# Kernel optimization log

Measured on AMD Instinct MI355X. Metric: run time of the kernel, lower is better.

The kernel has to match this reference:

```python
import jax, jax.numpy as jnp
import numpy as np

E, H = 1024, 16
B, N = 4, 2048
D = E // H

def setup_inputs() -> dict:
    key = jax.random.key(0)
    ks = jax.random.split(key, 5)
    s = 1.0 / np.sqrt(E)
    return {
        "x": jax.random.normal(ks[0], (B, N, E), dtype=jnp.float32),
        "Wqkv": jax.random.normal(ks[1], (E, 3 * E), dtype=jnp.float32) * s,
        "bqkv": jnp.zeros((3 * E,), dtype=jnp.float32),
        "Wproj": jax.random.normal(ks[2], (E, E), dtype=jnp.float32) * s,
        "bproj": jnp.zeros((E,), dtype=jnp.float32),
    }

def reference(x, Wqkv, bqkv, Wproj, bproj):
    b, n, e = x.shape
    qkv = x @ Wqkv + bqkv  # [b, n, 3e]
    # torch rearrange 'b n (h d qkv) -> qkv b h n d': last dim splits as (h, d, 3)
    qkv = qkv.reshape(b, n, H, D, 3)
    qkv = jnp.transpose(qkv, (4, 0, 2, 1, 3))  # [3, b, h, n, d]
    q, k, v = qkv[0], qkv[1], qkv[2]
    # NOTE: module scales by 1/sqrt(e) (full embed dim), faithfully reproduced
    att = jax.nn.softmax(jnp.einsum('bhqd,bhkd->bhqk', q, k) / jnp.sqrt(jnp.float32(E)), axis=-1)
    out = jnp.einsum('bhqk,bhkd->bhqd', att, v)  # dropout is identity in eval
    out = jnp.transpose(out, (0, 2, 1, 3)).reshape(b, n, e)  # 'b h n d -> b n (h d)'
    return out @ Wproj + bproj
```

## Files before the change

kernel.cpp:

```cpp
#include <hip/hip_runtime.h>
#include <stdint.h>

typedef unsigned short u16;
typedef __attribute__((ext_vector_type(8))) short short8;
typedef __attribute__((ext_vector_type(4))) float f32x4;

#define LOG2E 1.44269504088896340736f
#define CS (0.03125f * LOG2E)
#define BB 4
#define NN 2048
#define EE 1024
#define HH 16
#define DD 64
#define MM 8192
#define C3 3072

#if __has_builtin(__builtin_amdgcn_exp2f)
#define EXP2(x) __builtin_amdgcn_exp2f(x)
#else
#define EXP2(x) exp2f(x)
#endif

__device__ __forceinline__ u16 f2bf(float f) {
  union { float f; unsigned u; } v; v.f = f;
  unsigned r = v.u + 0x7fffu + ((v.u >> 16) & 1u);
  return (u16)(r >> 16);
}

#if __has_builtin(__builtin_amdgcn_cvt_pk_bf16_f32)
typedef __attribute__((ext_vector_type(2))) __bf16 bf16x2;
__device__ __forceinline__ unsigned pk2(float a, float b) {
  union { bf16x2 v; unsigned u; } c;
  c.v = __builtin_amdgcn_cvt_pk_bf16_f32(a, b);
  return c.u;
}
#else
__device__ __forceinline__ unsigned pk2(float a, float b) {
  union { float f; unsigned u; } x, y; x.f = a; y.f = b;
  return ((x.u + 0x8000u) >> 16) | ((y.u + 0x8000u) & 0xffff0000u);
}
#endif

__device__ __forceinline__ void async16(const void* g, void* l) {
  __builtin_amdgcn_global_load_lds((const __attribute__((address_space(1))) void*)g,
                                   (__attribute__((address_space(3))) void*)l,
                                   16, 0, 0);
}

__device__ __forceinline__ int vperm(int t) {
  return (t & 0x23) | ((t & 8) << 1) | ((t & 4) << 1) | ((t & 16) >> 2);
}

__global__ __launch_bounds__(256) void prep_kernel(const float* __restrict__ x, u16* __restrict__ xb,
                                                   const float* __restrict__ Wqkv, u16* __restrict__ WqkvT,
                                                   const float* __restrict__ Wproj, u16* __restrict__ WprojT) {
  __shared__ float tile[32][33];
  const int bid = blockIdx.x;
  if (bid < 8192) {
    int i = (bid * 256 + threadIdx.x) * 4;
    float4 v = *(const float4*)(x + i);
    ushort4 o; o.x = f2bf(v.x); o.y = f2bf(v.y); o.z = f2bf(v.z); o.w = f2bf(v.w);
    *(ushort4*)(xb + i) = o;
    return;
  }
  const int permute = bid < 11264 ? 1 : 0;
  const float* W = permute ? Wqkv : Wproj;
  u16* Wt = permute ? WqkvT : WprojT;
  const int ncols = permute ? C3 : EE;
  const int t = permute ? bid - 8192 : bid - 11264;
  const int nbx = permute ? 96 : 32;
  const int c0 = (t % nbx) * 32, k0 = (t / nbx) * 32;
  const int tx = threadIdx.x & 31, ty = threadIdx.x >> 5;
#pragma unroll
  for (int r = 0; r < 32; r += 8)
    tile[ty + r][tx] = W[(size_t)(k0 + ty + r) * ncols + c0 + tx];
  __syncthreads();
#pragma unroll
  for (int r = 0; r < 32; r += 8) {
    int c = c0 + ty + r;
    int cp = c;
    if (permute) {
      int tt = c % 3, hh = c / 192, d = (c / 3) % 64;
      cp = tt * 1024 + hh * 64 + d;
    }
    Wt[(size_t)cp * EE + k0 + tx] = f2bf(tile[tx][ty + r]);
  }
}

template <int KDIM>
__device__ __forceinline__ void gemm_core(const u16* __restrict__ A, const u16* __restrict__ Bt,
                                          int m0, int n0, u16* As, u16* Bs, f32x4 acc[4][4]) {
  const int tid = threadIdx.x;
  const int lane = tid & 63, wave = tid >> 6;
  const int q = lane >> 4, r16 = lane & 15;
  const int wrow = (wave >> 1) * 64, wcol = (wave & 1) * 64;
#pragma unroll
  for (int i = 0; i < 4; i++)
#pragma unroll
    for (int j = 0; j < 4; j++) acc[i][j] = (f32x4){0.f, 0.f, 0.f, 0.f};

  for (int k0 = 0; k0 < KDIM; k0 += 64) {
#pragma unroll
    for (int i = 0; i < 4; i++) {
      int c = i * 256 + tid;
      int ks = c >> 9, rem = c & 511, row = rem >> 2, k8 = rem & 3;
      async16(A + (size_t)(m0 + row) * KDIM + k0 + ks * 32 + k8 * 8, &As[c * 8]);
    }
#pragma unroll
    for (int i = 0; i < 4; i++) {
      int c = i * 256 + tid;
      int ks = c >> 9, rem = c & 511, row = rem >> 2, k8 = rem & 3;
      async16(Bt + (size_t)(n0 + row) * KDIM + k0 + ks * 32 + k8 * 8, &Bs[c * 8]);
    }
    __syncthreads();
#pragma unroll
    for (int ks = 0; ks < 2; ks++) {
      short8 af[4], bf[4];
#pragma unroll
      for (int i = 0; i < 4; i++)
        af[i] = *(const short8*)&As[ks * 4096 + (wrow + i * 16 + r16) * 32 + q * 8];
#pragma unroll
      for (int i = 0; i < 4; i++)
        bf[i] = *(const short8*)&Bs[ks * 4096 + (wcol + i * 16 + r16) * 32 + q * 8];
#pragma unroll
      for (int i = 0; i < 4; i++)
#pragma unroll
        for (int j = 0; j < 4; j++)
          acc[i][j] = __builtin_amdgcn_mfma_f32_16x16x32_bf16(af[i], bf[j], acc[i][j], 0, 0, 0);
    }
    __syncthreads();
  }
}

__global__ __launch_bounds__(256) void gemm_qkv(const u16* __restrict__ Xb, const u16* __restrict__ Wt,
                                                const float* __restrict__ bqkv, u16* __restrict__ Qb,
                                                u16* __restrict__ Kb, u16* __restrict__ Vt) {
  __shared__ __align__(16) u16 As[128 * 64];
  __shared__ __align__(16) u16 Bs[128 * 64];
  f32x4 acc[4][4];
  const int m0 = blockIdx.y * 128, n0 = blockIdx.x * 128;
  gemm_core<EE>(Xb, Wt, m0, n0, As, Bs, acc);
  const int tid = threadIdx.x, lane = tid & 63, wave = tid >> 6;
  const int q = lane >> 4, r16 = lane & 15;
  const int wrow = (wave >> 1) * 64, wcol = (wave & 1) * 64;
  const int t = (n0 + wcol) >> 10;
  const int b = (m0 + wrow) >> 11;
#pragma unroll
  for (int ci = 0; ci < 4; ci++) {
    const int cp = n0 + wcol + ci * 16 + r16;
    const int hh = (cp >> 6) & 15, d = cp & 63;
    const float bias = bqkv[hh * 192 + d * 3 + t];
    if (t == 0) {
#pragma unroll
      for (int ri = 0; ri < 4; ri++)
#pragma unroll
        for (int r = 0; r < 4; r++) {
          const int m = m0 + wrow + ri * 16 + q * 4 + r;
          Qb[((size_t)(b * 16 + hh) * 2048 + (m & 2047)) * 64 + d] = f2bf((acc[ri][ci][r] + bias) * CS);
        }
    } else if (t == 1) {
#pragma unroll
      for (int ri = 0; ri < 4; ri++)
#pragma unroll
        for (int r = 0; r < 4; r++) {
          const int m = m0 + wrow + ri * 16 + q * 4 + r;
          Kb[((size_t)(b * 16 + hh) * 2048 + (m & 2047)) * 64 + d] = f2bf(acc[ri][ci][r] + bias);
        }
    } else {
#pragma unroll
      for (int ri = 0; ri < 4; ri++) {
        const int nb = (m0 + wrow + ri * 16 + q * 4) & 2047;
        const int ns = (nb & ~63) + vperm(nb & 63);
        ushort4 w;
        w.x = f2bf(acc[ri][ci][0] + bias);
        w.y = f2bf(acc[ri][ci][1] + bias);
        w.z = f2bf(acc[ri][ci][2] + bias);
        w.w = f2bf(acc[ri][ci][3] + bias);
        *(ushort4*)&Vt[((size_t)(b * 16 + hh) * 64 + d) * 2048 + ns] = w;
      }
    }
  }
}

__global__ __launch_bounds__(256) void gemm_proj(const u16* __restrict__ Ob, const u16* __restrict__ Wt,
                                                 const float* __restrict__ bp, float* __restrict__ out) {
  __shared__ __align__(16) u16 As[128 * 64];
  __shared__ __align__(16) u16 Bs[128 * 64];
  f32x4 acc[4][4];
  const int m0 = blockIdx.y * 128, n0 = blockIdx.x * 128;
  gemm_core<EE>(Ob, Wt, m0, n0, As, Bs, acc);
  const int tid = threadIdx.x, lane = tid & 63, wave = tid >> 6;
  const int q = lane >> 4, r16 = lane & 15;
  const int wrow = (wave >> 1) * 64, wcol = (wave & 1) * 64;
#pragma unroll
  for (int ci = 0; ci < 4; ci++) {
    const int col = n0 + wcol + ci * 16 + r16;
    const float bias = bp[col];
#pragma unroll
    for (int ri = 0; ri < 4; ri++)
#pragma unroll
      for (int r = 0; r < 4; r++) {
        const int m = m0 + wrow + ri * 16 + q * 4 + r;
        out[(size_t)m * EE + col] = acc[ri][ci][r] + bias;
      }
  }
}

__global__ __launch_bounds__(256, 4) void attn_kernel(const u16* __restrict__ Qg, const u16* __restrict__ Kg,
                                                      const u16* __restrict__ Vg, u16* __restrict__ Ob) {
  __shared__ __align__(16) u16 Kd[2][4096];
  __shared__ __align__(16) u16 Vd[2][4096];
  const int tid = threadIdx.x, lane = tid & 63, wave = tid >> 6;
  const int q = lane >> 4, r16 = lane & 15;
  const int id = blockIdx.x + 16 * blockIdx.y;
  const int g = id & 7, s = id >> 3;
  const int bh = g * 8 + (s >> 4);
  const int q0 = (s & 15) * 128;
  const u16* Qp = Qg + ((size_t)bh * NN + q0) * DD;
  const u16* Kp = Kg + (size_t)bh * NN * DD;
  const u16* Vp = Vg + (size_t)bh * DD * NN;

  short8 qf[2][2];
#pragma unroll
  for (int nj = 0; nj < 2; nj++)
#pragma unroll
    for (int ks = 0; ks < 2; ks++)
      qf[nj][ks] = *(const short8*)(Qp + (wave * 32 + nj * 16 + r16) * 64 + ks * 32 + q * 8);

#pragma unroll
  for (int i = 0; i < 2; i++) {
    int c = i * 256 + tid;
    int ks = c >> 8, rem = c & 255, row = rem >> 2, k8 = rem & 3;
    async16(Kp + row * 64 + ks * 32 + k8 * 8, &Kd[0][c * 8]);
  }
#pragma unroll
  for (int i = 0; i < 2; i++) {
    int c = i * 256 + tid;
    int ks = c >> 8, rem = c & 255, d = rem >> 2, k8 = rem & 3;
    async16(Vp + d * NN + ks * 32 + k8 * 8, &Vd[0][c * 8]);
  }
  __syncthreads();

  f32x4 o[2][4];
  f32x4 ol[2];
#pragma unroll
  for (int i = 0; i < 2; i++) {
    ol[i] = (f32x4){0.f, 0.f, 0.f, 0.f};
#pragma unroll
    for (int j = 0; j < 4; j++) o[i][j] = (f32x4){0.f, 0.f, 0.f, 0.f};
  }
  const short8 ones = {16256, 16256, 16256, 16256, 16256, 16256, 16256, 16256};

  for (int j = 0; j < 32; j++) {
    const int buf = j & 1;
    if (j < 31) {
      const u16* Kt_ = Kp + (j + 1) * 64 * 64;
#pragma unroll
      for (int i = 0; i < 2; i++) {
        int c = i * 256 + tid;
        int ks = c >> 8, rem = c & 255, row = rem >> 2, k8 = rem & 3;
        async16(Kt_ + row * 64 + ks * 32 + k8 * 8, &Kd[buf ^ 1][c * 8]);
      }
#pragma unroll
      for (int i = 0; i < 2; i++) {
        int c = i * 256 + tid;
        int ks = c >> 8, rem = c & 255, d = rem >> 2, k8 = rem & 3;
        async16(Vp + d * NN + (j + 1) * 64 + ks * 32 + k8 * 8, &Vd[buf ^ 1][c * 8]);
      }
    }

    f32x4 st[4][2];
#pragma unroll
    for (int mi = 0; mi < 4; mi++)
#pragma unroll
      for (int nj = 0; nj < 2; nj++) st[mi][nj] = (f32x4){0.f, 0.f, 0.f, 0.f};
#pragma unroll
    for (int ks = 0; ks < 2; ks++) {
      short8 kf[4];
#pragma unroll
      for (int mi = 0; mi < 4; mi++)
        kf[mi] = *(const short8*)&Kd[buf][ks * 2048 + (mi * 16 + r16) * 32 + q * 8];
#pragma unroll
      for (int mi = 0; mi < 4; mi++)
#pragma unroll
        for (int nj = 0; nj < 2; nj++)
          st[mi][nj] = __builtin_amdgcn_mfma_f32_16x16x32_bf16(kf[mi], qf[nj][ks], st[mi][nj], 0, 0, 0);
    }

    uint2 pka[4][2];
#pragma unroll
    for (int mi = 0; mi < 4; mi++)
#pragma unroll
      for (int nj = 0; nj < 2; nj++) {
        float p0 = EXP2(st[mi][nj][0]);
        float p1 = EXP2(st[mi][nj][1]);
        float p2 = EXP2(st[mi][nj][2]);
        float p3 = EXP2(st[mi][nj][3]);
        pka[mi][nj].x = pk2(p0, p1);
        pka[mi][nj].y = pk2(p2, p3);
      }

#pragma unroll
    for (int kp = 0; kp < 2; kp++) {
      short8 vf[4];
#pragma unroll
      for (int ci = 0; ci < 4; ci++)
        vf[ci] = *(const short8*)&Vd[buf][kp * 2048 + (ci * 16 + r16) * 32 + q * 8];
#pragma unroll
      for (int ri = 0; ri < 2; ri++) {
        union { uint4 u; short8 s; } a;
        a.u.x = pka[2 * kp][ri].x;
        a.u.y = pka[2 * kp][ri].y;
        a.u.z = pka[2 * kp + 1][ri].x;
        a.u.w = pka[2 * kp + 1][ri].y;
#pragma unroll
        for (int ci = 0; ci < 4; ci++)
          o[ri][ci] = __builtin_amdgcn_mfma_f32_16x16x32_bf16(a.s, vf[ci], o[ri][ci], 0, 0, 0);
        ol[ri] = __builtin_amdgcn_mfma_f32_16x16x32_bf16(a.s, ones, ol[ri], 0, 0, 0);
      }
    }

    __syncthreads();
  }

  const int b = bh >> 4, h = bh & 15;
#pragma unroll
  for (int ri = 0; ri < 2; ri++)
#pragma unroll
    for (int r = 0; r < 4; r++) {
      const float inv = 1.0f / ol[ri][r];
      const int n = q0 + wave * 32 + ri * 16 + q * 4 + r;
#pragma unroll
      for (int ci = 0; ci < 4; ci++) {
        const int d = ci * 16 + r16;
        Ob[((size_t)(b * NN + n)) * EE + h * 64 + d] = f2bf(o[ri][ci][r] * inv);
      }
    }
}


extern "C" void kernel_launch(void* const* d_in, const int* in_sizes, int n_in,
                              void* d_out, int out_size, void* d_ws, size_t ws_size,
                              hipStream_t stream) {
  const float* x     = (const float*)d_in[0];
  const float* Wqkv  = (const float*)d_in[1];
  const float* bqkv  = (const float*)d_in[2];
  const float* Wproj = (const float*)d_in[3];
  const float* bproj = (const float*)d_in[4];
  float* out = (float*)d_out;
  char* ws = (char*)d_ws;

  u16* Xb     = (u16*)(ws);
  u16* Ob     = Xb;
  u16* Qb     = (u16*)(ws + (size_t)(16 << 20));
  u16* Kb     = (u16*)(ws + (size_t)(32 << 20));
  u16* Vt     = (u16*)(ws + (size_t)(48 << 20));
  u16* WqkvT  = (u16*)(ws + (size_t)(64 << 20));
  u16* WprojT = (u16*)(ws + (size_t)(72 << 20));

  prep_kernel<<<12288, 256, 0, stream>>>(x, Xb, Wqkv, WqkvT, Wproj, WprojT);
  gemm_qkv<<<dim3(24, 64), 256, 0, stream>>>(Xb, WqkvT, bqkv, Qb, Kb, Vt);
  attn_kernel<<<dim3(16, 64), 256, 0, stream>>>(Qb, Kb, Vt, Ob);
  gemm_proj<<<dim3(8, 64), 256, 0, stream>>>(Ob, WprojT, bproj, out);
}
```

Baseline: 270.8 us.

## Store K and V in interleaved MFMA-fragment tile layout for contiguous attention loads

The QKV GEMM epilogue now writes K and V into a single buffer where each 64-key tile holds K then V, pre-arranged in the exact per-lane fragment order the MFMA reads expect. The attention kernel then loads each tile with one fully contiguous 16 KB async copy and reads LDS fragments at lane*8 stride, replacing strided row gathers. This removes strided global reads and complex LDS indexing in the hot loop. The cost is scattered 2-byte stores for K in the GEMM epilogue, which may hurt write coalescing there.

```diff
diff --git a/kernel.cpp b/kernel.cpp
--- a/kernel.cpp
+++ b/kernel.cpp
@@ -132,9 +132,10 @@
   }
 }
 
+
 __global__ __launch_bounds__(256) void gemm_qkv(const u16* __restrict__ Xb, const u16* __restrict__ Wt,
                                                 const float* __restrict__ bqkv, u16* __restrict__ Qb,
-                                                u16* __restrict__ Kb, u16* __restrict__ Vt) {
+                                                u16* __restrict__ KVt) {
   __shared__ __align__(16) u16 As[128 * 64];
   __shared__ __align__(16) u16 Bs[128 * 64];
   f32x4 acc[4][4];
@@ -159,24 +160,30 @@
           Qb[((size_t)(b * 16 + hh) * 2048 + (m & 2047)) * 64 + d] = f2bf((acc[ri][ci][r] + bias) * CS);
         }
     } else if (t == 1) {
+      const size_t bhbase = (size_t)(b * 16 + hh) * 32;
+      const size_t dpart = (size_t)(d >> 5) * 2048 + ((d >> 3) & 3) * 128 + (d & 7);
 #pragma unroll
       for (int ri = 0; ri < 4; ri++)
 #pragma unroll
         for (int r = 0; r < 4; r++) {
-          const int m = m0 + wrow + ri * 16 + q * 4 + r;
-          Kb[((size_t)(b * 16 + hh) * 2048 + (m & 2047)) * 64 + d] = f2bf(acc[ri][ci][r] + bias);
+          const int key = (m0 + wrow + ri * 16 + q * 4 + r) & 2047;
+          KVt[(bhbase + (key >> 6)) * 8192 + dpart + ((key >> 4) & 3) * 512 + (key & 15) * 8] =
+              f2bf(acc[ri][ci][r] + bias);
         }
     } else {
+      const size_t bhbase = (size_t)(b * 16 + hh) * 32;
+      const int dpart = (d >> 4) * 512 + (d & 15) * 8;
 #pragma unroll
       for (int ri = 0; ri < 4; ri++) {
         const int nb = (m0 + wrow + ri * 16 + q * 4) & 2047;
-        const int ns = (nb & ~63) + vperm(nb & 63);
+        const int sb = vperm(nb & 63);
         ushort4 w;
         w.x = f2bf(acc[ri][ci][0] + bias);
         w.y = f2bf(acc[ri][ci][1] + bias);
         w.z = f2bf(acc[ri][ci][2] + bias);
         w.w = f2bf(acc[ri][ci][3] + bias);
-        *(ushort4*)&Vt[((size_t)(b * 16 + hh) * 64 + d) * 2048 + ns] = w;
+        *(ushort4*)&KVt[(bhbase + (nb >> 6)) * 8192 + 4096 + (sb >> 5) * 2048 +
+                        ((sb >> 3) & 3) * 128 + dpart + (sb & 7)] = w;
       }
     }
   }
@@ -206,10 +213,9 @@
   }
 }
 
-__global__ __launch_bounds__(256, 4) void attn_kernel(const u16* __restrict__ Qg, const u16* __restrict__ Kg,
-                                                      const u16* __restrict__ Vg, u16* __restrict__ Ob) {
-  __shared__ __align__(16) u16 Kd[2][4096];
-  __shared__ __align__(16) u16 Vd[2][4096];
+__global__ __launch_bounds__(256, 4) void attn_kernel(const u16* __restrict__ Qg, const u16* __restrict__ KVg,
+                                                      u16* __restrict__ Ob) {
+  __shared__ __align__(16) u16 KVd[2][8192];
   const int tid = threadIdx.x, lane = tid & 63, wave = tid >> 6;
   const int q = lane >> 4, r16 = lane & 15;
   const int id = blockIdx.x + 16 * blockIdx.y;
@@ -217,8 +223,7 @@
   const int bh = g * 8 + (s >> 4);
   const int q0 = (s & 15) * 128;
   const u16* Qp = Qg + ((size_t)bh * NN + q0) * DD;
-  const u16* Kp = Kg + (size_t)bh * NN * DD;
-  const u16* Vp = Vg + (size_t)bh * DD * NN;
+  const u16* KVp = KVg + (size_t)bh * (32 * 8192);
 
   short8 qf[2][2];
 #pragma unroll
@@ -228,16 +233,9 @@
       qf[nj][ks] = *(const short8*)(Qp + (wave * 32 + nj * 16 + r16) * 64 + ks * 32 + q * 8);
 
 #pragma unroll
-  for (int i = 0; i < 2; i++) {
+  for (int i = 0; i < 4; i++) {
     int c = i * 256 + tid;
-    int ks = c >> 8, rem = c & 255, row = rem >> 2, k8 = rem & 3;
-    async16(Kp + row * 64 + ks * 32 + k8 * 8, &Kd[0][c * 8]);
-  }
-#pragma unroll
-  for (int i = 0; i < 2; i++) {
-    int c = i * 256 + tid;
-    int ks = c >> 8, rem = c & 255, d = rem >> 2, k8 = rem & 3;
-    async16(Vp + d * NN + ks * 32 + k8 * 8, &Vd[0][c * 8]);
+    async16(KVp + c * 8, &KVd[0][c * 8]);
   }
   __syncthreads();
 
@@ -254,18 +252,11 @@
   for (int j = 0; j < 32; j++) {
     const int buf = j & 1;
     if (j < 31) {
-      const u16* Kt_ = Kp + (j + 1) * 64 * 64;
-#pragma unroll
-      for (int i = 0; i < 2; i++) {
+      const u16* src = KVp + (size_t)(j + 1) * 8192;
+#pragma unroll
+      for (int i = 0; i < 4; i++) {
         int c = i * 256 + tid;
-        int ks = c >> 8, rem = c & 255, row = rem >> 2, k8 = rem & 3;
-        async16(Kt_ + row * 64 + ks * 32 + k8 * 8, &Kd[buf ^ 1][c * 8]);
-      }
-#pragma unroll
-      for (int i = 0; i < 2; i++) {
-        int c = i * 256 + tid;
-        int ks = c >> 8, rem = c & 255, d = rem >> 2, k8 = rem & 3;
-        async16(Vp + d * NN + (j + 1) * 64 + ks * 32 + k8 * 8, &Vd[buf ^ 1][c * 8]);
+        async16(src + c * 8, &KVd[buf ^ 1][c * 8]);
       }
     }
 
@@ -279,7 +270,7 @@
       short8 kf[4];
 #pragma unroll
       for (int mi = 0; mi < 4; mi++)
-        kf[mi] = *(const short8*)&Kd[buf][ks * 2048 + (mi * 16 + r16) * 32 + q * 8];
+        kf[mi] = *(const short8*)&KVd[buf][ks * 2048 + mi * 512 + lane * 8];
 #pragma unroll
       for (int mi = 0; mi < 4; mi++)
 #pragma unroll
@@ -305,7 +296,7 @@
       short8 vf[4];
 #pragma unroll
       for (int ci = 0; ci < 4; ci++)
-        vf[ci] = *(const short8*)&Vd[buf][kp * 2048 + (ci * 16 + r16) * 32 + q * 8];
+        vf[ci] = *(const short8*)&KVd[buf][4096 + kp * 2048 + ci * 512 + lane * 8];
 #pragma unroll
       for (int ri = 0; ri < 2; ri++) {
         union { uint4 u; short8 s; } a;
@@ -353,13 +344,12 @@
   u16* Xb     = (u16*)(ws);
   u16* Ob     = Xb;
   u16* Qb     = (u16*)(ws + (size_t)(16 << 20));
-  u16* Kb     = (u16*)(ws + (size_t)(32 << 20));
-  u16* Vt     = (u16*)(ws + (size_t)(48 << 20));
+  u16* KVt    = (u16*)(ws + (size_t)(32 << 20));
   u16* WqkvT  = (u16*)(ws + (size_t)(64 << 20));
   u16* WprojT = (u16*)(ws + (size_t)(72 << 20));
 
   prep_kernel<<<12288, 256, 0, stream>>>(x, Xb, Wqkv, WqkvT, Wproj, WprojT);
-  gemm_qkv<<<dim3(24, 64), 256, 0, stream>>>(Xb, WqkvT, bqkv, Qb, Kb, Vt);
-  attn_kernel<<<dim3(16, 64), 256, 0, stream>>>(Qb, Kb, Vt, Ob);
+  gemm_qkv<<<dim3(24, 64), 256, 0, stream>>>(Xb, WqkvT, bqkv, Qb, KVt);
+  attn_kernel<<<dim3(16, 64), 256, 0, stream>>>(Qb, KVt, Ob);
   gemm_proj<<<dim3(8, 64), 256, 0, stream>>>(Ob, WprojT, bproj, out);
 }
```

After: 276.7 us. +2.2%, slower.
